# Kernel tuning notes

Measured on AMD Instinct MI355X. Metric: run time of the kernel, lower is better.

## Reference

```python
import jax, jax.numpy as jnp
import numpy as np

B, N, IN_F, OUT_F, REL_DIM, NUM_REL = 4, 2048, 256, 128, 10, 6
D = OUT_F // 2  # internal_dim
ALPHA = 0.2
LAMBDA_INIT = 0.8 - 0.6 * float(np.exp(-0.3 * 1))  # depth=1
EPS = 1e-5


def setup_inputs() -> dict:
    key = jax.random.key(0)
    ks = jax.random.split(key, 16)
    return {
        "h": jax.random.normal(ks[0], (B, N, IN_F), jnp.float32),
        "adj": jax.random.randint(ks[1], (B, N, N), 0, NUM_REL, jnp.int32),
        "W": jax.random.normal(ks[2], (IN_F, OUT_F), jnp.float32) * (1.414 / np.sqrt(IN_F)),
        "a_left_pos": jax.random.normal(ks[3], (D,), jnp.float32) * 0.1,
        "a_right_pos": jax.random.normal(ks[4], (D,), jnp.float32) * 0.1,
        "a_left_neg": jax.random.normal(ks[5], (D,), jnp.float32) * 0.1,
        "a_right_neg": jax.random.normal(ks[6], (D,), jnp.float32) * 0.1,
        "rel_emb": jax.random.normal(ks[7], (NUM_REL, REL_DIM), jnp.float32),
        "a_rel_pos": jax.random.normal(ks[8], (REL_DIM,), jnp.float32) * 0.3,
        "a_rel_neg": jax.random.normal(ks[9], (REL_DIM,), jnp.float32) * 0.3,
        "lambda_left1": jax.random.normal(ks[10], (D,), jnp.float32) * 0.1,
        "lambda_right1": jax.random.normal(ks[11], (D,), jnp.float32) * 0.1,
        "lambda_left2": jax.random.normal(ks[12], (D,), jnp.float32) * 0.1,
        "lambda_right2": jax.random.normal(ks[13], (D,), jnp.float32) * 0.1,
        "ln_gamma": jnp.ones((OUT_F,), jnp.float32),
        "ln_beta": jnp.zeros((OUT_F,), jnp.float32),
    }


def _leaky_relu(x):
    return jnp.where(x >= 0, x, ALPHA * x)


def reference(h, adj, W, a_left_pos, a_right_pos, a_left_neg, a_right_neg,
              rel_emb, a_rel_pos, a_rel_neg,
              lambda_left1, lambda_right1, lambda_left2, lambda_right2,
              ln_gamma, ln_beta):
    Wh = jnp.einsum('bnf,fo->bno', h, W)              # [B,N,OUT_F]
    Wh4 = Wh.reshape(B, N, 2, D)
    Wh_pos, Wh_neg = Wh4[:, :, 0, :], Wh4[:, :, 1, :]  # [B,N,D]

    # e[b,i,j] = left[b,i] + right[b,j] + rel_score[adj[b,i,j]]
    # relation Linear(rel_dim,1) applied to embedding rows == per-relation scalar lookup
    rel_score_pos = rel_emb @ a_rel_pos               # [NUM_REL]
    rel_score_neg = rel_emb @ a_rel_neg
    e_pos = (Wh_pos @ a_left_pos)[:, :, None] + (Wh_pos @ a_right_pos)[:, None, :] + rel_score_pos[adj]
    e_neg = (Wh_neg @ a_left_neg)[:, :, None] + (Wh_neg @ a_right_neg)[:, None, :] + rel_score_neg[adj]

    neg_inf = jnp.float32(-9e15)
    mask = adj > 0
    attn_pos = jax.nn.softmax(jnp.where(mask, _leaky_relu(e_pos), neg_inf), axis=2)
    attn_neg = jax.nn.softmax(jnp.where(mask, _leaky_relu(e_neg), neg_inf), axis=2)

    lam1 = jnp.exp(jnp.sum(lambda_left1 * lambda_right1))
    lam2 = jnp.exp(jnp.sum(lambda_left2 * lambda_right2))
    lambda_full = lam1 - lam2 + LAMBDA_INIT
    attention = attn_pos - lambda_full * attn_neg     # [B,N,N]

    Wh_v = jnp.concatenate([Wh_pos, Wh_neg], axis=-1)  # [B,N,OUT_F]
    h_prime = jnp.einsum('bij,bjo->bio', attention, Wh_v)

    mu = jnp.mean(h_prime, axis=-1, keepdims=True)
    var = jnp.mean(jnp.square(h_prime - mu), axis=-1, keepdims=True)
    h_prime = (h_prime - mu) * jax.lax.rsqrt(var + EPS) * ln_gamma + ln_beta
    h_prime = h_prime * (1.0 - LAMBDA_INIT)
    return jax.nn.gelu(h_prime, approximate=False), attention
```

## Files before the change

kernel.cpp:

```cpp
#include <hip/hip_runtime.h>
#include <math.h>

typedef short bf16x8 __attribute__((ext_vector_type(8)));
typedef float f32x4  __attribute__((ext_vector_type(4)));

constexpr int   B_    = 4;
constexpr int   N_    = 2048;
constexpr int   INF_  = 256;
constexpr int   OUTF_ = 128;
constexpr float LAMBDA_INIT_ = 0.35550906759096926f;
constexpr float OUT_SCALE_   = 0.64449093240903074f;
constexpr float EPS_         = 1e-5f;
constexpr float LOG2E_       = 1.44269504088896340736f;

__device__ inline unsigned short f2bf(float x) {
  unsigned u = __float_as_uint(x);
  u += 0x7fffu + ((u >> 16) & 1u);
  return (unsigned short)(u >> 16);
}
__device__ inline unsigned pack2(float a, float b) {
  return (unsigned)f2bf(a) | ((unsigned)f2bf(b) << 16);
}

__global__ void scalars_kernel(const float* __restrict__ rel_emb,
                               const float* __restrict__ a_rel_pos,
                               const float* __restrict__ a_rel_neg,
                               const float* __restrict__ ll1, const float* __restrict__ lr1,
                               const float* __restrict__ ll2, const float* __restrict__ lr2,
                               float* __restrict__ scal) {
  int lane = threadIdx.x;
  float p1 = ll1[lane] * lr1[lane];
  float p2 = ll2[lane] * lr2[lane];
  #pragma unroll
  for (int off = 32; off; off >>= 1) { p1 += __shfl_xor(p1, off); p2 += __shfl_xor(p2, off); }
  if (lane == 0) scal[12] = expf(p1) - expf(p2) + LAMBDA_INIT_;
  if (lane < 6) {
    float sp = 0.f, sn = 0.f;
    for (int k = 0; k < 10; ++k) {
      float rv = rel_emb[lane * 10 + k];
      sp += rv * a_rel_pos[k];
      sn += rv * a_rel_neg[k];
    }
    scal[lane]     = sp * LOG2E_;
    scal[6 + lane] = sn * LOG2E_;
  }
}

__global__ __launch_bounds__(256) void wh_dots_kernel(
    const float* __restrict__ h, const float* __restrict__ W,
    const float* __restrict__ alp, const float* __restrict__ arp,
    const float* __restrict__ aln, const float* __restrict__ arn,
    unsigned short* __restrict__ WhvT,
    float* __restrict__ lposv, float* __restrict__ rposv,
    float* __restrict__ lnegv, float* __restrict__ rnegv) {
  __shared__ __align__(16) float hT[INF_][20];
  const int t = threadIdx.x;
  const size_t row0 = (size_t)blockIdx.x * 16;
  #pragma unroll
  for (int i = 0; i < 16; ++i) hT[t][i] = h[(row0 + i) * INF_ + t];
  __syncthreads();
  const int c  = t & 127;
  const int rg = t >> 7;
  float acc[8] = {0.f, 0.f, 0.f, 0.f, 0.f, 0.f, 0.f, 0.f};
  #pragma unroll 4
  for (int k = 0; k < INF_; ++k) {
    float wv = W[k * OUTF_ + c];
    const float4* hp = reinterpret_cast<const float4*>(&hT[k][rg * 8]);
    float4 h0 = hp[0], h1 = hp[1];
    acc[0] += h0.x * wv; acc[1] += h0.y * wv; acc[2] += h0.z * wv; acc[3] += h0.w * wv;
    acc[4] += h1.x * wv; acc[5] += h1.y * wv; acc[6] += h1.z * wv; acc[7] += h1.w * wv;
  }
  uint4 pk;
  pk.x = pack2(acc[0], acc[1]); pk.y = pack2(acc[2], acc[3]);
  pk.z = pack2(acc[4], acc[5]); pk.w = pack2(acc[6], acc[7]);
  const int b  = (int)(row0 >> 11);
  const int n0 = (int)(row0 & 2047) + rg * 8;
  *reinterpret_cast<uint4*>(WhvT + ((size_t)b * OUTF_ + c) * N_ + n0) = pk;

  const int lane = t & 63;
  const int wv   = t >> 6;
  const bool pos = (wv & 1) == 0;
  const float al = pos ? alp[lane] : aln[lane];
  const float ar = pos ? arp[lane] : arn[lane];
  float sl[8], sr2[8];
  #pragma unroll
  for (int r = 0; r < 8; ++r) { sl[r] = acc[r] * al; sr2[r] = acc[r] * ar; }
  #pragma unroll
  for (int off = 32; off; off >>= 1) {
    #pragma unroll
    for (int r = 0; r < 8; ++r) {
      sl[r]  += __shfl_xor(sl[r],  off);
      sr2[r] += __shfl_xor(sr2[r], off);
    }
  }
  if (lane == 0) {
    #pragma unroll
    for (int r = 0; r < 8; ++r) {
      const int node = (int)row0 + rg * 8 + r;
      if (pos) { lposv[node] = sl[r] * LOG2E_; rposv[node] = sr2[r] * LOG2E_; }
      else     { lnegv[node] = sl[r] * LOG2E_; rnegv[node] = sr2[r] * LOG2E_; }
    }
  }
}

__global__ __launch_bounds__(512) void attn_v4(
    const int* __restrict__ adj,
    const float* __restrict__ lposv, const float* __restrict__ rposv,
    const float* __restrict__ lnegv, const float* __restrict__ rnegv,
    const float* __restrict__ scal, float* __restrict__ out1) {
  __shared__ float sums[2][16];
  const int t = threadIdx.x;
  const int lane = t & 63;
  const int wv = t >> 6;
  const int flat0 = blockIdx.x * 8;
  const int b = flat0 >> 11;

  const float lam = scal[12];
  float srcP = -1.0e30f, srcN = -1.0e30f;
  if (lane >= 1 && lane <= 5) { srcP = scal[lane]; srcN = scal[6 + lane]; }
  const int iSrcP = __float_as_int(srcP);
  const int iSrcN = __float_as_int(srcN);

  const int j0 = t * 4;
  float4 rp4 = *reinterpret_cast<const float4*>(rposv + b * N_ + j0);
  float4 rn4 = *reinterpret_cast<const float4*>(rnegv + b * N_ + j0);
  const float rp[4] = {rp4.x, rp4.y, rp4.z, rp4.w};
  const float rn[4] = {rn4.x, rn4.y, rn4.z, rn4.w};

  int4 avN = *reinterpret_cast<const int4*>(adj + (size_t)flat0 * N_ + j0);

  #pragma unroll
  for (int r = 0; r < 8; ++r) {
    const int flat = flat0 + r;
    const int4 av4 = avN;
    if (r < 7)
      avN = *reinterpret_cast<const int4*>(adj + (size_t)(flat + 1) * N_ + j0);
    const float lP = lposv[flat];
    const float lN = lnegv[flat];
    int av[4] = {av4.x, av4.y, av4.z, av4.w};

    float p[4], n[4];
    #pragma unroll
    for (int q = 0; q < 4; ++q) {
      float rsp = __int_as_float(__builtin_amdgcn_ds_bpermute(av[q] << 2, iSrcP));
      float rsn = __int_as_float(__builtin_amdgcn_ds_bpermute(av[q] << 2, iSrcN));
      float e  = lP + rp[q] + rsp;
      float en = lN + rn[q] + rsn;
      e  = fmaxf(e, 0.2f * e);
      en = fmaxf(en, 0.2f * en);
      p[q] = __builtin_amdgcn_exp2f(e);
      n[q] = __builtin_amdgcn_exp2f(en);
    }
    float sP = (p[0] + p[1]) + (p[2] + p[3]);
    float sN = (n[0] + n[1]) + (n[2] + n[3]);
    #pragma unroll
    for (int off = 32; off; off >>= 1) { sP += __shfl_xor(sP, off); sN += __shfl_xor(sN, off); }
    const int bf = r & 1;
    if (lane == 0) { sums[bf][wv] = sP; sums[bf][8 + wv] = sN; }
    __syncthreads();
    float vP = sums[bf][lane & 7];
    vP += __shfl_xor(vP, 1); vP += __shfl_xor(vP, 2); vP += __shfl_xor(vP, 4);
    float vN = sums[bf][8 + (lane & 7)];
    vN += __shfl_xor(vN, 1); vN += __shfl_xor(vN, 2); vN += __shfl_xor(vN, 4);
    const float s1 = 1.f / vP;
    const float s2 = -lam / vN;

    float a[4];
    #pragma unroll
    for (int q = 0; q < 4; ++q) a[q] = p[q] * s1 + n[q] * s2;
    float* o1 = out1 + (size_t)flat * N_ + j0;
    *reinterpret_cast<float4*>(o1) = make_float4(a[0], a[1], a[2], a[3]);
  }
}

__global__ __launch_bounds__(512, 4) void pv_v5c(
    const float* __restrict__ attn, const unsigned short* __restrict__ WhvT,
    const float* __restrict__ gamma, const float* __restrict__ beta,
    float* __restrict__ out0) {
  __shared__ __align__(16) uint4 A4[2][16 * 32];
  __shared__ __align__(16) float hp[16][132];
  const int t = threadIdx.x;
  const int lane = t & 63;
  const int w = t >> 6;
  const int bi = blockIdx.x;
  const int b  = bi >> 7;
  const int i0 = (bi & 127) * 16;

  const int sr = t >> 5;
  const int sj = t & 31;
  const float4* src4 = reinterpret_cast<const float4*>(
      attn + ((size_t)(b * N_ + i0 + sr)) * N_ + sj * 8);
  const int swz = sr & 7;
  const int ui = sr * 32 + (sj ^ swz);

  const int bl  = lane & 15;
  const int kg  = lane >> 4;
  const int ch  = w * 16 + bl;
  const unsigned short* Bp = WhvT + ((size_t)b * OUTF_ + ch) * N_ + kg * 8;
  f32x4 acc0 = {0.f, 0.f, 0.f, 0.f};
  f32x4 acc1 = {0.f, 0.f, 0.f, 0.f};
  const int arow = bl * 32;
  const int aswz = bl & 7;

  bf16x8 bBuf[2][8];

  {
    float4 s0 = src4[0], s1 = src4[1];
    uint4 u;
    u.x = pack2(s0.x, s0.y); u.y = pack2(s0.z, s0.w);
    u.z = pack2(s1.x, s1.y); u.w = pack2(s1.z, s1.w);
    A4[0][ui] = u;
  }
  float4 n0 = src4[64], n1 = src4[65];
  #pragma unroll
  for (int kk = 0; kk < 8; ++kk)
    bBuf[0][kk] = *reinterpret_cast<const bf16x8*>(Bp + kk * 32);
  __syncthreads();

  #pragma unroll
  for (int c = 0; c < 8; ++c) {
    const int cur = c & 1;
    float4 m0, m1;
    if (c < 6) { m0 = src4[(c + 2) * 64]; m1 = src4[(c + 2) * 64 + 1]; }
    if (c < 7) {
      #pragma unroll
      for (int kk = 0; kk < 8; ++kk)
        bBuf[cur ^ 1][kk] = *reinterpret_cast<const bf16x8*>(Bp + (c + 1) * 256 + kk * 32);
    }
    #pragma unroll
    for (int kk = 0; kk < 8; ++kk) {
      bf16x8 a = *reinterpret_cast<const bf16x8*>(&A4[cur][arow + ((kk * 4 + kg) ^ aswz)]);
      if (cur == 0) acc0 = __builtin_amdgcn_mfma_f32_16x16x32_bf16(a, bBuf[0][kk], acc0, 0, 0, 0);
      else          acc1 = __builtin_amdgcn_mfma_f32_16x16x32_bf16(a, bBuf[1][kk], acc1, 0, 0, 0);
    }
    if (c < 7) {
      uint4 u;
      u.x = pack2(n0.x, n0.y); u.y = pack2(n0.z, n0.w);
      u.z = pack2(n1.x, n1.y); u.w = pack2(n1.z, n1.w);
      A4[cur ^ 1][ui] = u;
    }
    n0 = m0; n1 = m1;
    __syncthreads();
  }

  #pragma unroll
  for (int q = 0; q < 4; ++q) hp[kg * 4 + q][ch] = acc0[q] + acc1[q];
  __syncthreads();

  const int row = t >> 5;
  const int c0  = t & 31;
  float v[4], s = 0.f, sq = 0.f;
  #pragma unroll
  for (int e = 0; e < 4; ++e) {
    v[e] = hp[row][c0 + e * 32];
    s += v[e]; sq += v[e] * v[e];
  }
  #pragma unroll
  for (int off = 16; off; off >>= 1) { s += __shfl_xor(s, off); sq += __shfl_xor(sq, off); }
  const float mu  = s  * (1.f / 128.f);
  const float var = sq * (1.f / 128.f) - mu * mu;
  const float inv = rsqrtf(var + EPS_);
  float* orow = out0 + ((size_t)(b * N_ + i0 + row)) * OUTF_;
  #pragma unroll
  for (int e = 0; e < 4; ++e) {
    const int chh = c0 + e * 32;
    float y = (v[e] - mu) * inv * gamma[chh] + beta[chh];
    y *= OUT_SCALE_;
    orow[chh] = 0.5f * y * (1.f + erff(y * 0.70710678118654752f));
  }
}

extern "C" void kernel_launch(void* const* d_in, const int* in_sizes, int n_in,
                              void* d_out, int out_size, void* d_ws, size_t ws_size,
                              hipStream_t stream) {
  (void)in_sizes; (void)n_in; (void)out_size; (void)ws_size;
  const float* h        = (const float*)d_in[0];
  const int*   adj      = (const int*)d_in[1];
  const float* W        = (const float*)d_in[2];
  const float* alp      = (const float*)d_in[3];
  const float* arp      = (const float*)d_in[4];
  const float* aln      = (const float*)d_in[5];
  const float* arn      = (const float*)d_in[6];
  const float* rel_emb  = (const float*)d_in[7];
  const float* a_rel_p  = (const float*)d_in[8];
  const float* a_rel_n  = (const float*)d_in[9];
  const float* ll1      = (const float*)d_in[10];
  const float* lr1      = (const float*)d_in[11];
  const float* ll2      = (const float*)d_in[12];
  const float* lr2      = (const float*)d_in[13];
  const float* gamma    = (const float*)d_in[14];
  const float* beta     = (const float*)d_in[15];

  float* out0 = (float*)d_out;
  float* out1 = out0 + (size_t)B_ * N_ * OUTF_;

  float* ws    = (float*)d_ws;
  float* scal  = ws;
  float* lposv = ws + 32;
  float* rposv = lposv + B_ * N_;
  float* lnegv = rposv + B_ * N_;
  float* rnegv = lnegv + B_ * N_;
  unsigned short* WhvT = (unsigned short*)(rnegv + B_ * N_);

  scalars_kernel<<<1, 64, 0, stream>>>(rel_emb, a_rel_p, a_rel_n, ll1, lr1, ll2, lr2, scal);
  wh_dots_kernel<<<(B_ * N_) / 16, 256, 0, stream>>>(h, W, alp, arp, aln, arn,
                                                     WhvT, lposv, rposv, lnegv, rnegv);
  attn_v4<<<(B_ * N_) / 8, 512, 0, stream>>>(adj, lposv, rposv, lnegv, rnegv, scal, out1);
  pv_v5c<<<B_ * (N_ / 16), 512, 0, stream>>>(out1, WhvT, gamma, beta, out0);
}
```

Measured before the change: 90.81 us.

## Fuse attention softmax and PV matmul into one kernel via shared-memory staging

Merges the attention-computation kernel and the attention-times-values matmul kernel into a single kernel that processes 16 rows per block. Each block writes the attention rows to the output and also packs them as bf16 into shared memory, then runs the MFMA matmul and layernorm/GELU from shared memory. This removes the second kernel's full re-read of the fp32 attention matrix from global memory. In exchange it uses a large shared-memory buffer per block, which lowers occupancy, and it serializes the softmax and matmul phases within each block.

```diff
diff --git a/kernel.cpp b/kernel.cpp
--- a/kernel.cpp
+++ b/kernel.cpp
@@ -103,17 +103,24 @@
   }
 }
 
-__global__ __launch_bounds__(512) void attn_v4(
+__global__ __launch_bounds__(512, 4) void fused_attn_pv(
     const int* __restrict__ adj,
     const float* __restrict__ lposv, const float* __restrict__ rposv,
     const float* __restrict__ lnegv, const float* __restrict__ rnegv,
-    const float* __restrict__ scal, float* __restrict__ out1) {
-  __shared__ float sums[2][16];
+    const float* __restrict__ scal, const unsigned short* __restrict__ WhvT,
+    const float* __restrict__ gamma, const float* __restrict__ beta,
+    float* __restrict__ out0, float* __restrict__ out1) {
+  __shared__ __align__(16) uint4 A4[16 * 256];
+  float* scr = reinterpret_cast<float*>(&A4[15 * 256]);
+  float (*hp)[132] = reinterpret_cast<float (*)[132]>(A4);
+
   const int t = threadIdx.x;
   const int lane = t & 63;
   const int wv = t >> 6;
-  const int flat0 = blockIdx.x * 8;
-  const int b = flat0 >> 11;
+  const int bi = blockIdx.x;
+  const int b  = bi >> 7;
+  const int i0 = (bi & 127) * 16;
+  const int flat0 = b * N_ + i0;
 
   const float lam = scal[12];
   float srcP = -1.0e30f, srcN = -1.0e30f;
@@ -127,13 +134,15 @@
   const float rp[4] = {rp4.x, rp4.y, rp4.z, rp4.w};
   const float rn[4] = {rn4.x, rn4.y, rn4.z, rn4.w};
 
+  const int wchunk = (t >> 1) >> 5;
+  const int wloc   = (t >> 1) & 31;
+
   int4 avN = *reinterpret_cast<const int4*>(adj + (size_t)flat0 * N_ + j0);
 
-  #pragma unroll
-  for (int r = 0; r < 8; ++r) {
+  for (int r = 0; r < 16; ++r) {
     const int flat = flat0 + r;
     const int4 av4 = avN;
-    if (r < 7)
+    if (r < 15)
       avN = *reinterpret_cast<const int4*>(adj + (size_t)(flat + 1) * N_ + j0);
     const float lP = lposv[flat];
     const float lN = lnegv[flat];
@@ -156,11 +165,11 @@
     #pragma unroll
     for (int off = 32; off; off >>= 1) { sP += __shfl_xor(sP, off); sN += __shfl_xor(sN, off); }
     const int bf = r & 1;
-    if (lane == 0) { sums[bf][wv] = sP; sums[bf][8 + wv] = sN; }
+    if (lane == 0) { scr[bf * 16 + wv] = sP; scr[bf * 16 + 8 + wv] = sN; }
     __syncthreads();
-    float vP = sums[bf][lane & 7];
+    float vP = scr[bf * 16 + (lane & 7)];
     vP += __shfl_xor(vP, 1); vP += __shfl_xor(vP, 2); vP += __shfl_xor(vP, 4);
-    float vN = sums[bf][8 + (lane & 7)];
+    float vN = scr[bf * 16 + 8 + (lane & 7)];
     vN += __shfl_xor(vN, 1); vN += __shfl_xor(vN, 2); vN += __shfl_xor(vN, 4);
     const float s1 = 1.f / vP;
     const float s2 = -lam / vN;
@@ -170,58 +179,32 @@
     for (int q = 0; q < 4; ++q) a[q] = p[q] * s1 + n[q] * s2;
     float* o1 = out1 + (size_t)flat * N_ + j0;
     *reinterpret_cast<float4*>(o1) = make_float4(a[0], a[1], a[2], a[3]);
-  }
-}
-
-__global__ __launch_bounds__(512, 4) void pv_v5c(
-    const float* __restrict__ attn, const unsigned short* __restrict__ WhvT,
-    const float* __restrict__ gamma, const float* __restrict__ beta,
-    float* __restrict__ out0) {
-  __shared__ __align__(16) uint4 A4[2][16 * 32];
-  __shared__ __align__(16) float hp[16][132];
-  const int t = threadIdx.x;
-  const int lane = t & 63;
-  const int w = t >> 6;
-  const int bi = blockIdx.x;
-  const int b  = bi >> 7;
-  const int i0 = (bi & 127) * 16;
-
-  const int sr = t >> 5;
-  const int sj = t & 31;
-  const float4* src4 = reinterpret_cast<const float4*>(
-      attn + ((size_t)(b * N_ + i0 + sr)) * N_ + sj * 8);
-  const int swz = sr & 7;
-  const int ui = sr * 32 + (sj ^ swz);
+
+    if (r == 15) __syncthreads();
+    const int uidx = r * 256 + wchunk * 32 + (wloc ^ (r & 7));
+    uint2 val;
+    val.x = pack2(a[0], a[1]); val.y = pack2(a[2], a[3]);
+    reinterpret_cast<uint2*>(A4)[uidx * 2 + (t & 1)] = val;
+  }
+  __syncthreads();
 
   const int bl  = lane & 15;
   const int kg  = lane >> 4;
-  const int ch  = w * 16 + bl;
+  const int ch  = wv * 16 + bl;
   const unsigned short* Bp = WhvT + ((size_t)b * OUTF_ + ch) * N_ + kg * 8;
   f32x4 acc0 = {0.f, 0.f, 0.f, 0.f};
   f32x4 acc1 = {0.f, 0.f, 0.f, 0.f};
-  const int arow = bl * 32;
+  const int arow = bl * 256;
   const int aswz = bl & 7;
 
   bf16x8 bBuf[2][8];
-
-  {
-    float4 s0 = src4[0], s1 = src4[1];
-    uint4 u;
-    u.x = pack2(s0.x, s0.y); u.y = pack2(s0.z, s0.w);
-    u.z = pack2(s1.x, s1.y); u.w = pack2(s1.z, s1.w);
-    A4[0][ui] = u;
-  }
-  float4 n0 = src4[64], n1 = src4[65];
   #pragma unroll
   for (int kk = 0; kk < 8; ++kk)
     bBuf[0][kk] = *reinterpret_cast<const bf16x8*>(Bp + kk * 32);
-  __syncthreads();
 
   #pragma unroll
   for (int c = 0; c < 8; ++c) {
     const int cur = c & 1;
-    float4 m0, m1;
-    if (c < 6) { m0 = src4[(c + 2) * 64]; m1 = src4[(c + 2) * 64 + 1]; }
     if (c < 7) {
       #pragma unroll
       for (int kk = 0; kk < 8; ++kk)
@@ -229,19 +212,12 @@
     }
     #pragma unroll
     for (int kk = 0; kk < 8; ++kk) {
-      bf16x8 a = *reinterpret_cast<const bf16x8*>(&A4[cur][arow + ((kk * 4 + kg) ^ aswz)]);
+      bf16x8 a = *reinterpret_cast<const bf16x8*>(&A4[arow + c * 32 + ((kk * 4 + kg) ^ aswz)]);
       if (cur == 0) acc0 = __builtin_amdgcn_mfma_f32_16x16x32_bf16(a, bBuf[0][kk], acc0, 0, 0, 0);
       else          acc1 = __builtin_amdgcn_mfma_f32_16x16x32_bf16(a, bBuf[1][kk], acc1, 0, 0, 0);
     }
-    if (c < 7) {
-      uint4 u;
-      u.x = pack2(n0.x, n0.y); u.y = pack2(n0.z, n0.w);
-      u.z = pack2(n1.x, n1.y); u.w = pack2(n1.z, n1.w);
-      A4[cur ^ 1][ui] = u;
-    }
-    n0 = m0; n1 = m1;
-    __syncthreads();
-  }
+  }
+  __syncthreads();
 
   #pragma unroll
   for (int q = 0; q < 4; ++q) hp[kg * 4 + q][ch] = acc0[q] + acc1[q];
@@ -305,6 +281,6 @@
   scalars_kernel<<<1, 64, 0, stream>>>(rel_emb, a_rel_p, a_rel_n, ll1, lr1, ll2, lr2, scal);
   wh_dots_kernel<<<(B_ * N_) / 16, 256, 0, stream>>>(h, W, alp, arp, aln, arn,
                                                      WhvT, lposv, rposv, lnegv, rnegv);
-  attn_v4<<<(B_ * N_) / 8, 512, 0, stream>>>(adj, lposv, rposv, lnegv, rnegv, scal, out1);
-  pv_v5c<<<B_ * (N_ / 16), 512, 0, stream>>>(out1, WhvT, gamma, beta, out0);
-}
+  fused_attn_pv<<<B_ * (N_ / 16), 512, 0, stream>>>(adj, lposv, rposv, lnegv, rnegv,
+                                                    scal, WhvT, gamma, beta, out0, out1);
+}
```

New measurement: 89.39 us. About the same (-1.6%).
